# Kernel optimization log

Measured on AMD Instinct MI355X. Metric: run time of the kernel, lower is better.

## Reference

```python
import jax, jax.numpy as jnp
import numpy as np

N = 100000
E = 3200000

def gcn_conv(x, W, b, src, dst, num_nodes):
    # PyG GCNConv: x' = D^-1/2 (A+I) D^-1/2 (x W) + b
    h = x @ W  # [N, out]
    # self loops appended
    src_sl = jnp.concatenate([src, jnp.arange(num_nodes)])
    dst_sl = jnp.concatenate([dst, jnp.arange(num_nodes)])
    deg = jnp.zeros((num_nodes,), h.dtype).at[dst_sl].add(1.0)
    dinv = jnp.where(deg > 0, 1.0 / jnp.sqrt(deg), 0.0)
    norm = dinv[src_sl] * dinv[dst_sl]  # [E+N]
    msgs = h[src_sl] * norm[:, None]
    out = jnp.zeros_like(h).at[dst_sl].add(msgs)
    return out + b

def setup_inputs() -> dict:
    key = jax.random.key(0)
    k1, k2, k3, k4, k5 = jax.random.split(key, 5)
    z = jax.random.normal(k1, (N, 16), dtype=jnp.float32)
    edge_index = jax.random.randint(k2, (2, E), 0, N, dtype=jnp.int64)
    W1 = jax.random.normal(k3, (16, 256), dtype=jnp.float32) * (1.0 / np.sqrt(16))
    b1 = jnp.zeros((256,), jnp.float32)
    W2 = jax.random.normal(k4, (256, 256), dtype=jnp.float32) * (1.0 / np.sqrt(256))
    b2 = jnp.zeros((256,), jnp.float32)
    return {"z": z, "edge_index": edge_index, "W1": W1, "b1": b1, "W2": W2, "b2": b2}

def reference(z, edge_index, W1, b1, W2, b2):
    src, dst = edge_index[0], edge_index[1]
    h = gcn_conv(z, W1, b1, src, dst, N)
    h = gcn_conv(h, W2, b2, src, dst, N)
    value = jnp.sum(h[src] * h[dst], axis=1)  # [E]
    return jax.nn.sigmoid(value)
```

## Files before the change

kernel.cpp:

```cpp
#include <hip/hip_runtime.h>
#include <hip/hip_fp16.h>
#include <math.h>

#define N_NODES 100000
#define N_EDGES 3200000
#define GRID_N 391
#define GRID_G 6250
#define NSB 782
#define SB_NODES 128
#define SBCAP 5120
#define E_BLK 12800
#define PART_BLOCKS 250
#define PART_THREADS 1024
#define GRID_DEC 12500

#define OFF_DINV 0
#define OFF_C    100016
#define OFF_ZS16 200032
#define OFF_T16  1000048
#define OFF_U    1800064
#define OFF_YT   3400080
#define OFF_ST   4200080
#define OFF_PR   6604720
#define OFF_PB   6604736
#define OFF_ABG  6604752
#define OFF_L    6604768
#define FLOAT_TOTAL 6605024
#define IOFF_GCUR 0
#define IOFF_BEG  1024
#define IOFF_CNT  101024
#define IOFF_BUF  201024
#define IOFF_CSR  4204864

__device__ inline float4 h4_to_f4(uint2 v) {
    __half2 a = *reinterpret_cast<__half2*>(&v.x);
    __half2 b = *reinterpret_cast<__half2*>(&v.y);
    float2 fa = __half22float2(a), fb = __half22float2(b);
    return make_float4(fa.x, fa.y, fb.x, fb.y);
}
__device__ inline uint2 f4_to_h4(float4 f) {
    uint2 r;
    __half2 a = __floats2half2_rn(f.x, f.y);
    __half2 b = __floats2half2_rn(f.z, f.w);
    r.x = *reinterpret_cast<unsigned*>(&a);
    r.y = *reinterpret_cast<unsigned*>(&b);
    return r;
}
__device__ inline float4 pack_h8(float4 a, float4 b) {
    float4 r;
    __half2* p = reinterpret_cast<__half2*>(&r);
    p[0] = __floats2half2_rn(a.x, a.y);
    p[1] = __floats2half2_rn(a.z, a.w);
    p[2] = __floats2half2_rn(b.x, b.y);
    p[3] = __floats2half2_rn(b.z, b.w);
    return r;
}
__device__ inline unsigned h2bits(float a, float b) {
    __half2 h = __floats2half2_rn(a, b);
    return *reinterpret_cast<unsigned*>(&h);
}
__device__ inline float2 bits2f2(unsigned v) {
    __half2 h = *reinterpret_cast<__half2*>(&v);
    return __half22float2(h);
}
__device__ inline float hdot8f(float4 a, float4 b) {
    const __half2* pa = reinterpret_cast<const __half2*>(&a);
    const __half2* pb = reinterpret_cast<const __half2*>(&b);
    float s = 0.0f;
    #pragma unroll
    for (int i = 0; i < 4; i++) {
        float2 fa = __half22float2(pa[i]);
        float2 fb = __half22float2(pb[i]);
        s += fa.x * fb.x + fa.y * fb.y;
    }
    return s;
}
__device__ inline void acc4(float4& acc, uint2 g) {
    float4 f = h4_to_f4(g);
    acc.x += f.x; acc.y += f.y; acc.z += f.z; acc.w += f.w;
}

struct ConstsSh {
    float sW1t[16 * 256];
    float sM[16 * 257];
    float sb1[256];
    float sb2[256];
    float sR[256];
    float sG[256];
    float sLf[256];
};
struct PartSh {
    int hist[4][NSB];
    int cur[NSB];
};

__global__ void __launch_bounds__(PART_THREADS)
k_part(const int* __restrict__ src, const int* __restrict__ dst,
       int* __restrict__ gcur, int* __restrict__ buf,
       const float* __restrict__ W1, const float* __restrict__ b1,
       const float* __restrict__ W2, const float* __restrict__ b2,
       float* __restrict__ ws) {
    __shared__ union { ConstsSh c; PartSh p; } sh;
    int t = threadIdx.x;

    if (blockIdx.x == PART_BLOCKS) {
        bool act = t < 256;
        if (act) {
            #pragma unroll
            for (int r = 0; r < 16; r++)
                sh.c.sW1t[t * 16 + r] = W1[r * 256 + t];
            sh.c.sb1[t] = b1[t];
            sh.c.sb2[t] = b2[t];
        }
        __syncthreads();
        if (act) {
            float acc[16];
            #pragma unroll
            for (int i = 0; i < 16; i++) acc[i] = 0.0f;
            float raccv = 0.0f;
            for (int kk = 0; kk < 256; kk += 8) {
                float w2v[8];
                #pragma unroll
                for (int u = 0; u < 8; u++)
                    w2v[u] = W2[(kk + u) * 256 + t];
                #pragma unroll
                for (int u = 0; u < 8; u++) {
                    #pragma unroll
                    for (int i = 0; i < 16; i++)
                        acc[i] += sh.c.sW1t[(kk + u) * 16 + i] * w2v[u];
                    raccv += sh.c.sb1[kk + u] * w2v[u];
                }
            }
            #pragma unroll
            for (int i = 0; i < 16; i++) sh.c.sM[i * 257 + t] = acc[i];
            sh.c.sR[t] = raccv;
        }
        __syncthreads();
        if (act) {
            int i = t >> 4, j = t & 15;
            float gg = 0.0f;
            for (int tt = 0; tt < 256; tt++)
                gg += sh.c.sM[i * 257 + tt] * sh.c.sM[j * 257 + tt];
            sh.c.sG[t] = gg;
        }
        if (t < 16) {
            float a = 0.0f, b = 0.0f;
            for (int tt = 0; tt < 256; tt++) {
                a += sh.c.sM[t * 257 + tt] * sh.c.sR[tt];
                b += sh.c.sM[t * 257 + tt] * sh.c.sb2[tt];
            }
            ws[OFF_PR + t] = a;
            ws[OFF_PB + t] = b;
        }
        if (t == 0) {
            float al = 0.0f, be = 0.0f, ga = 0.0f;
            for (int tt = 0; tt < 256; tt++) {
                al += sh.c.sR[tt] * sh.c.sR[tt];
                be += sh.c.sR[tt] * sh.c.sb2[tt];
                ga += sh.c.sb2[tt] * sh.c.sb2[tt];
            }
            float disc = sqrtf(al * al + 4.0f);
            float lp = 0.5f * (al + disc);
            float lm = 0.5f * (al - disc);
            float k1 = sqrtf(lp / (lp * lp + 1.0f));
            float k2 = sqrtf(-lm / (lm * lm + 1.0f));
            ws[OFF_ABG + 0] = be;
            ws[OFF_ABG + 1] = 0.5f * ga;
            ws[OFF_ABG + 2] = lp;
            ws[OFF_ABG + 3] = lm;
            ws[OFF_ABG + 4] = k1;
            ws[OFF_ABG + 5] = k2;
        }
        __syncthreads();
        if (act) sh.c.sLf[t] = 0.0f;
        __syncthreads();
        for (int j = 0; j < 16; j++) {
            if (t == j) {
                float s = sh.c.sG[j * 16 + j];
                for (int k = 0; k < j; k++)
                    s -= sh.c.sLf[j * 16 + k] * sh.c.sLf[j * 16 + k];
                sh.c.sLf[j * 16 + j] = sqrtf(fmaxf(s, 1e-20f));
            }
            __syncthreads();
            if (t > j && t < 16) {
                float s = sh.c.sG[t * 16 + j];
                for (int k = 0; k < j; k++)
                    s -= sh.c.sLf[t * 16 + k] * sh.c.sLf[j * 16 + k];
                sh.c.sLf[t * 16 + j] = s / sh.c.sLf[j * 16 + j];
            }
            __syncthreads();
        }
        if (act) ws[OFF_L + t] = sh.c.sLf[t];
        return;
    }

    int cp = t >> 8;
    int base = blockIdx.x * E_BLK;
    for (int i = t; i < 4 * NSB; i += PART_THREADS) ((int*)sh.p.hist)[i] = 0;
    __syncthreads();
    for (int i = t; i < E_BLK; i += PART_THREADS) {
        int e = base + i;
        if (e < N_EDGES)
            atomicAdd(&sh.p.hist[cp][__builtin_nontemporal_load(dst + e) >> 7], 1);
    }
    __syncthreads();
    for (int i = t; i < NSB; i += PART_THREADS) {
        int h = sh.p.hist[0][i] + sh.p.hist[1][i] + sh.p.hist[2][i] + sh.p.hist[3][i];
        sh.p.cur[i] = (h > 0) ? atomicAdd(&gcur[i], h) : 0;
    }
    __syncthreads();
    for (int i = t; i < E_BLK; i += PART_THREADS) {
        int e = base + i;
        if (e >= N_EDGES) continue;
        int d = __builtin_nontemporal_load(dst + e);
        int s = __builtin_nontemporal_load(src + e);
        int sb = d >> 7;
        int pos = atomicAdd(&sh.p.cur[sb], 1);
        if (pos < SBCAP) buf[sb * SBCAP + pos] = s | ((d & 127) << 17);
    }
}

__global__ void k_sort(const float* __restrict__ z, const int* __restrict__ gcur,
                       const int* __restrict__ buf, int* __restrict__ csr,
                       int* __restrict__ begA, int* __restrict__ cntA,
                       float* __restrict__ ws) {
    __shared__ int pay[SBCAP];
    __shared__ int h[SB_NODES + 1];
    __shared__ int lcur[SB_NODES];
    __shared__ float sdv[SB_NODES];
    int sb = blockIdx.x, t = threadIdx.x;
    int n = gcur[sb];
    if (n > SBCAP) n = SBCAP;
    for (int i = t; i < n; i += 256) pay[i] = buf[sb * SBCAP + i];
    if (t <= SB_NODES) h[t] = 0;
    __syncthreads();
    for (int i = t; i < n; i += 256) atomicAdd(&h[(pay[i] >> 17) + 1], 1);
    __syncthreads();
    int mydeg = 0;
    if (t < SB_NODES) { mydeg = h[t + 1]; h[t + 1] = (mydeg + 3) & ~3; }
    __syncthreads();
    for (int off = 1; off <= SB_NODES; off <<= 1) {
        int v = 0;
        if (t <= SB_NODES && t >= off) v = h[t - off];
        __syncthreads();
        if (t <= SB_NODES) h[t] += v;
        __syncthreads();
    }
    int n0 = sb * SB_NODES;
    if (t < SB_NODES) {
        lcur[t] = h[t];
        float dv = rsqrtf((float)(mydeg + 1));
        sdv[t] = dv;
        if (n0 + t < N_NODES) {
            cntA[n0 + t] = mydeg;
            begA[n0 + t] = sb * SBCAP + h[t];
            ws[OFF_DINV + n0 + t] = dv;
        }
    }
    __syncthreads();
    {
        int nl = t >> 1, half = t & 1;
        int node = n0 + nl;
        if (node < N_NODES) {
            const float4* zr = (const float4*)(z + (size_t)node * 16) + 2 * half;
            float dv = sdv[nl];
            float4 a = zr[0], b = zr[1];
            a = make_float4(a.x * dv, a.y * dv, a.z * dv, a.w * dv);
            b = make_float4(b.x * dv, b.y * dv, b.z * dv, b.w * dv);
            ((float4*)((__half*)(ws + OFF_ZS16) + (size_t)node * 16))[half] = pack_h8(a, b);
        }
    }
    for (int i = t; i < n; i += 256) {
        int p = pay[i];
        int dl = p >> 17;
        int pos = atomicAdd(&lcur[dl], 1);
        if (pos < SBCAP) csr[sb * SBCAP + pos] = p & 0x1FFFF;
    }
}

__global__ void k_gather1(const int* __restrict__ cntA, const int* __restrict__ begA,
                          const int* __restrict__ csr, float* __restrict__ ws) {
    int lane = threadIdx.x & 15;
    int g = threadIdx.x >> 4;
    int q = lane & 3;
    int sub = lane >> 2;
    int d = blockIdx.x * 16 + g;
    if (d >= N_NODES) return;
    const float* dinv = ws + OFF_DINV;
    const __half* zs = (const __half*)(ws + OFF_ZS16);
    float dd = dinv[d];
    float dv2 = dd * dd;
    int deg = cntA[d];
    int beg = begA[d];
    float4 acc = make_float4(0.f, 0.f, 0.f, 0.f);
    float csum = 0.0f;
    int j = 0;
    for (; j + 32 <= deg; j += 32) {
        int4 ia = *(const int4*)(csr + beg + j + sub * 4);
        int4 ib = *(const int4*)(csr + beg + j + 16 + sub * 4);
        uint2 g0 = ((const uint2*)(zs + (size_t)ia.x * 16))[q];
        uint2 g1 = ((const uint2*)(zs + (size_t)ia.y * 16))[q];
        uint2 g2 = ((const uint2*)(zs + (size_t)ia.z * 16))[q];
        uint2 g3 = ((const uint2*)(zs + (size_t)ia.w * 16))[q];
        uint2 g4 = ((const uint2*)(zs + (size_t)ib.x * 16))[q];
        uint2 g5 = ((const uint2*)(zs + (size_t)ib.y * 16))[q];
        uint2 g6 = ((const uint2*)(zs + (size_t)ib.z * 16))[q];
        uint2 g7 = ((const uint2*)(zs + (size_t)ib.w * 16))[q];
        float dva = 0.0f, dvb = 0.0f;
        if (q == 0) {
            dva = (dinv[ia.x] + dinv[ia.y]) + (dinv[ia.z] + dinv[ia.w]);
            dvb = (dinv[ib.x] + dinv[ib.y]) + (dinv[ib.z] + dinv[ib.w]);
        }
        __builtin_amdgcn_sched_barrier(0);
        acc4(acc, g0); acc4(acc, g1); acc4(acc, g2); acc4(acc, g3);
        acc4(acc, g4); acc4(acc, g5); acc4(acc, g6); acc4(acc, g7);
        csum += dva + dvb;
    }
    for (; j + 16 <= deg; j += 16) {
        int4 idx = *(const int4*)(csr + beg + j + sub * 4);
        uint2 g0 = ((const uint2*)(zs + (size_t)idx.x * 16))[q];
        uint2 g1 = ((const uint2*)(zs + (size_t)idx.y * 16))[q];
        uint2 g2 = ((const uint2*)(zs + (size_t)idx.z * 16))[q];
        uint2 g3 = ((const uint2*)(zs + (size_t)idx.w * 16))[q];
        acc4(acc, g0); acc4(acc, g1); acc4(acc, g2); acc4(acc, g3);
        if (q == 0) csum += (dinv[idx.x] + dinv[idx.y]) + (dinv[idx.z] + dinv[idx.w]);
    }
    for (int t = j + sub; t < deg; t += 4) {
        int s0 = csr[beg + t];
        acc4(acc, ((const uint2*)(zs + (size_t)s0 * 16))[q]);
        if (q == 0) csum += dinv[s0];
    }
    #pragma unroll
    for (int off = 4; off <= 8; off <<= 1) {
        acc.x += __shfl_xor(acc.x, off, 64);
        acc.y += __shfl_xor(acc.y, off, 64);
        acc.z += __shfl_xor(acc.z, off, 64);
        acc.w += __shfl_xor(acc.w, off, 64);
        csum  += __shfl_xor(csum,  off, 64);
    }
    if (sub == 0) {
        float4 zrow = h4_to_f4(((const uint2*)(zs + (size_t)d * 16))[q]);
        float4 o = make_float4(dv2 * (acc.x + zrow.x), dv2 * (acc.y + zrow.y),
                               dv2 * (acc.z + zrow.z), dv2 * (acc.w + zrow.w));
        ((uint2*)((__half*)(ws + OFF_T16) + (size_t)d * 16))[q] = f4_to_h4(o);
        if (q == 0) (ws + OFF_C)[d] = dd * csum + dv2;
    }
}

__global__ void k_gather2(const int* __restrict__ cntA, const int* __restrict__ begA,
                          const int* __restrict__ csr, float* __restrict__ ws) {
    int lane = threadIdx.x & 15;
    int g = threadIdx.x >> 4;
    int q = lane & 3;
    int sub = lane >> 2;
    int d = blockIdx.x * 16 + g;
    if (d >= N_NODES) return;
    const float* dinv = ws + OFF_DINV;
    const __half* t16 = (const __half*)(ws + OFF_T16);
    float dd = dinv[d];
    int deg = cntA[d];
    int beg = begA[d];
    float4 acc = make_float4(0.f, 0.f, 0.f, 0.f);
    int j = 0;
    for (; j + 32 <= deg; j += 32) {
        int4 ia = *(const int4*)(csr + beg + j + sub * 4);
        int4 ib = *(const int4*)(csr + beg + j + 16 + sub * 4);
        uint2 g0 = ((const uint2*)(t16 + (size_t)ia.x * 16))[q];
        uint2 g1 = ((const uint2*)(t16 + (size_t)ia.y * 16))[q];
        uint2 g2 = ((const uint2*)(t16 + (size_t)ia.z * 16))[q];
        uint2 g3 = ((const uint2*)(t16 + (size_t)ia.w * 16))[q];
        uint2 g4 = ((const uint2*)(t16 + (size_t)ib.x * 16))[q];
        uint2 g5 = ((const uint2*)(t16 + (size_t)ib.y * 16))[q];
        uint2 g6 = ((const uint2*)(t16 + (size_t)ib.z * 16))[q];
        uint2 g7 = ((const uint2*)(t16 + (size_t)ib.w * 16))[q];
        __builtin_amdgcn_sched_barrier(0);
        acc4(acc, g0); acc4(acc, g1); acc4(acc, g2); acc4(acc, g3);
        acc4(acc, g4); acc4(acc, g5); acc4(acc, g6); acc4(acc, g7);
    }
    for (; j + 16 <= deg; j += 16) {
        int4 idx = *(const int4*)(csr + beg + j + sub * 4);
        uint2 g0 = ((const uint2*)(t16 + (size_t)idx.x * 16))[q];
        uint2 g1 = ((const uint2*)(t16 + (size_t)idx.y * 16))[q];
        uint2 g2 = ((const uint2*)(t16 + (size_t)idx.z * 16))[q];
        uint2 g3 = ((const uint2*)(t16 + (size_t)idx.w * 16))[q];
        acc4(acc, g0); acc4(acc, g1); acc4(acc, g2); acc4(acc, g3);
    }
    for (int t = j + sub; t < deg; t += 4) {
        int s0 = csr[beg + t];
        acc4(acc, ((const uint2*)(t16 + (size_t)s0 * 16))[q]);
    }
    #pragma unroll
    for (int off = 4; off <= 8; off <<= 1) {
        acc.x += __shfl_xor(acc.x, off, 64);
        acc.y += __shfl_xor(acc.y, off, 64);
        acc.z += __shfl_xor(acc.z, off, 64);
        acc.w += __shfl_xor(acc.w, off, 64);
    }
    if (sub == 0) {
        float4 trow = h4_to_f4(((const uint2*)(t16 + (size_t)d * 16))[q]);
        float4 o = make_float4(dd * (acc.x + trow.x), dd * (acc.y + trow.y),
                               dd * (acc.z + trow.z), dd * (acc.w + trow.w));
        ((float4*)(ws + OFF_U + (size_t)d * 16))[q] = o;
    }
}

__global__ void k_pack(float* __restrict__ ws) {
    __shared__ float sL[256];
    __shared__ float spr[16];
    __shared__ float spb[16];
    __shared__ float sprm[8];
    int tid = threadIdx.x;
    sL[tid] = ws[OFF_L + tid];
    if (tid < 16) { spr[tid] = ws[OFF_PR + tid]; spb[tid] = ws[OFF_PB + tid]; }
    if (tid < 8) sprm[tid] = ws[OFF_ABG + tid];
    __syncthreads();
    int i = blockIdx.x * blockDim.x + tid;
    if (i >= N_NODES) return;
    const float* u = ws + OFF_U;
    const float* c = ws + OFF_C;
    float ur[16];
    const float4* urow = (const float4*)(u + (size_t)i * 16);
    #pragma unroll
    for (int m = 0; m < 4; m++) {
        float4 a = urow[m];
        ur[4 * m + 0] = a.x; ur[4 * m + 1] = a.y;
        ur[4 * m + 2] = a.z; ur[4 * m + 3] = a.w;
    }
    float A = 0.0f, B = 0.0f;
    #pragma unroll
    for (int kk = 0; kk < 16; kk++) { A += ur[kk] * spr[kk]; B += ur[kk] * spb[kk]; }
    float y[16];
    #pragma unroll
    for (int j = 0; j < 16; j++) {
        float accv = 0.0f;
        #pragma unroll
        for (int kk = 0; kk < 16; kk++) accv += ur[kk] * sL[kk * 16 + j];
        y[j] = accv;
    }
    float beta = sprm[0], gh = sprm[1], lp = sprm[2], lm = sprm[3];
    float k1 = sprm[4], k2 = sprm[5];
    float ci = c[i];
    float Ap = A + beta;
    float Bp = B + gh;
    float r1 = k1 * (lp * ci + Ap);
    float r2 = k2 * (lm * ci + Ap);
    const float inv_s2 = 0.70710678118654752f;
    float r3 = (Bp + 1.0f) * inv_s2;
    float r4 = (Bp - 1.0f) * inv_s2;
    float4* yt = (float4*)(ws + OFF_YT);
    yt[2 * i]     = pack_h8(make_float4(y[0], y[1], y[2], y[3]),
                            make_float4(y[4], y[5], y[6], y[7]));
    yt[2 * i + 1] = pack_h8(make_float4(y[8], y[9], y[10], y[11]),
                            make_float4(y[12], y[13], y[14], y[15]));
    ((uint2*)(ws + OFF_ST))[i] = make_uint2(h2bits(r1, r2), h2bits(r3, r4));
}

__global__ void k_decode(const int* __restrict__ src, const int* __restrict__ dst,
                         const float* __restrict__ ws, float* __restrict__ out) {
    int e = blockIdx.x * 256 + threadIdx.x;
    const float4* yt = (const float4*)(ws + OFF_YT);
    const uint2*  st = (const uint2*)(ws + OFF_ST);
    int s = __builtin_nontemporal_load(src + e);
    int d = __builtin_nontemporal_load(dst + e);
    float4 sy0 = yt[2 * (size_t)s];
    float4 sy1 = yt[2 * (size_t)s + 1];
    float4 dy0 = yt[2 * (size_t)d];
    float4 dy1 = yt[2 * (size_t)d + 1];
    uint2  ssc = st[s];
    uint2  dsc = st[d];
    __builtin_amdgcn_sched_barrier(0);
    float v = hdot8f(sy0, dy0) + hdot8f(sy1, dy1);
    float2 ra = bits2f2(ssc.x), rb = bits2f2(dsc.x);
    float2 rc = bits2f2(ssc.y), rd = bits2f2(dsc.y);
    v += ra.x * rb.x - ra.y * rb.y + rc.x * rd.x - rc.y * rd.y;
    __builtin_nontemporal_store(1.0f / (1.0f + expf(-v)), out + e);
}

extern "C" void kernel_launch(void* const* d_in, const int* in_sizes, int n_in,
                              void* d_out, int out_size, void* d_ws, size_t ws_size,
                              hipStream_t stream) {
    const float* z  = (const float*)d_in[0];
    const int*   ei = (const int*)d_in[1];
    const float* W1 = (const float*)d_in[2];
    const float* b1 = (const float*)d_in[3];
    const float* W2 = (const float*)d_in[4];
    const float* b2 = (const float*)d_in[5];
    float* out = (float*)d_out;
    float* ws  = (float*)d_ws;
    int*   wi  = (int*)(ws + FLOAT_TOTAL);

    const int* src = ei;
    const int* dst = ei + N_EDGES;

    int* gcur = wi + IOFF_GCUR;
    int* begA = wi + IOFF_BEG;
    int* cntA = wi + IOFF_CNT;
    int* buf  = wi + IOFF_BUF;
    int* csr  = wi + IOFF_CSR;

    hipMemsetAsync(gcur, 0, 1024 * sizeof(int), stream);
    k_part    <<<PART_BLOCKS + 1, PART_THREADS, 0, stream>>>(src, dst, gcur, buf,
                                                             W1, b1, W2, b2, ws);
    k_sort    <<<NSB, 256, 0, stream>>>(z, gcur, buf, csr, begA, cntA, ws);
    k_gather1 <<<GRID_G, 256, 0, stream>>>(cntA, begA, csr, ws);
    k_gather2 <<<GRID_G, 256, 0, stream>>>(cntA, begA, csr, ws);
    k_pack    <<<GRID_N, 256, 0, stream>>>(ws);
    k_decode  <<<GRID_DEC, 256, 0, stream>>>(src, dst, ws, out);
}
```

Baseline: 284.0 us.

## Stage partitioned edges in LDS via local counting sort before global write

The edge-partition kernel now handles its edge block in two chunks. Each chunk is bucket-sorted into shared memory using a histogram, a block-wide prefix scan and atomic scatter. The sorted payload is then copied to the global bucket buffers in contiguous runs, with a binary search mapping each element to its bucket. This replaces fully scattered 4-byte global writes with more coalesced per-bucket writes. The cost is extra scan passes, barriers, per-element binary searches and a second chunk iteration.

```diff
diff --git a/kernel.cpp b/kernel.cpp
--- a/kernel.cpp
+++ b/kernel.cpp
@@ -10,6 +10,7 @@
 #define SB_NODES 128
 #define SBCAP 5120
 #define E_BLK 12800
+#define CH_E 6400
 #define PART_BLOCKS 250
 #define PART_THREADS 1024
 #define GRID_DEC 12500
@@ -90,8 +91,10 @@
     float sLf[256];
 };
 struct PartSh {
-    int hist[4][NSB];
-    int cur[NSB];
+    int h2[2][NSB];
+    int pref[NSB + 1];
+    int gbase[NSB];
+    int pay[CH_E];
 };
 
 __global__ void __launch_bounds__(PART_THREADS)
@@ -194,29 +197,57 @@
         return;
     }
 
-    int cp = t >> 8;
-    int base = blockIdx.x * E_BLK;
-    for (int i = t; i < 4 * NSB; i += PART_THREADS) ((int*)sh.p.hist)[i] = 0;
-    __syncthreads();
-    for (int i = t; i < E_BLK; i += PART_THREADS) {
-        int e = base + i;
-        if (e < N_EDGES)
-            atomicAdd(&sh.p.hist[cp][__builtin_nontemporal_load(dst + e) >> 7], 1);
-    }
-    __syncthreads();
-    for (int i = t; i < NSB; i += PART_THREADS) {
-        int h = sh.p.hist[0][i] + sh.p.hist[1][i] + sh.p.hist[2][i] + sh.p.hist[3][i];
-        sh.p.cur[i] = (h > 0) ? atomicAdd(&gcur[i], h) : 0;
-    }
-    __syncthreads();
-    for (int i = t; i < E_BLK; i += PART_THREADS) {
-        int e = base + i;
-        if (e >= N_EDGES) continue;
-        int d = __builtin_nontemporal_load(dst + e);
-        int s = __builtin_nontemporal_load(src + e);
-        int sb = d >> 7;
-        int pos = atomicAdd(&sh.p.cur[sb], 1);
-        if (pos < SBCAP) buf[sb * SBCAP + pos] = s | ((d & 127) << 17);
+    int cp = t >> 9;
+    for (int chunk = 0; chunk < 2; chunk++) {
+        int cbase = blockIdx.x * E_BLK + chunk * CH_E;
+        for (int i = t; i < 2 * NSB; i += PART_THREADS) ((int*)sh.p.h2)[i] = 0;
+        __syncthreads();
+        for (int i = t; i < CH_E; i += PART_THREADS) {
+            int e = cbase + i;
+            if (e < N_EDGES)
+                atomicAdd(&sh.p.h2[cp][__builtin_nontemporal_load(dst + e) >> 7], 1);
+        }
+        __syncthreads();
+        if (t == 0) sh.p.pref[0] = 0;
+        if (t < NSB) sh.p.pref[t + 1] = sh.p.h2[0][t] + sh.p.h2[1][t];
+        __syncthreads();
+        for (int off = 1; off <= NSB; off <<= 1) {
+            int v = 0;
+            if (t <= NSB && t >= off) v = sh.p.pref[t - off];
+            __syncthreads();
+            if (t <= NSB) sh.p.pref[t] += v;
+            __syncthreads();
+        }
+        for (int i = t; i < CH_E; i += PART_THREADS) {
+            int e = cbase + i;
+            if (e >= N_EDGES) continue;
+            int d = __builtin_nontemporal_load(dst + e);
+            int s = __builtin_nontemporal_load(src + e);
+            int sb = d >> 7;
+            int pos = atomicAdd(&sh.p.pref[sb], 1);
+            sh.p.pay[pos] = s | ((d & 127) << 17);
+        }
+        __syncthreads();
+        if (t < NSB) {
+            int end   = sh.p.pref[t];
+            int start = (t == 0) ? 0 : sh.p.pref[t - 1];
+            int cnt   = end - start;
+            sh.p.gbase[t] = (cnt > 0) ? atomicAdd(&gcur[t], cnt) : 0;
+        }
+        __syncthreads();
+        int tot = sh.p.pref[NSB];
+        for (int k = t; k < tot; k += PART_THREADS) {
+            int lo = 0, hi = NSB - 1;
+            while (lo < hi) {
+                int mid = (lo + hi) >> 1;
+                if (sh.p.pref[mid] > k) hi = mid; else lo = mid + 1;
+            }
+            int sb  = lo;
+            int ofs = k - ((sb == 0) ? 0 : sh.p.pref[sb - 1]);
+            int p   = sh.p.gbase[sb] + ofs;
+            if (p < SBCAP) buf[sb * SBCAP + p] = sh.p.pay[k];
+        }
+        __syncthreads();
     }
 }
 
```

Measured after the change: 281.3 us. About the same (-0.9%).
